# Kernel tuning notes

Measured on AMD Instinct MI355X. Metric: run time of the kernel, lower is better.

Reference implementation:

```python
import jax, jax.numpy as jnp
import numpy as np

B, S, E, R = 64, 2048, 256, 50


def setup_inputs() -> dict:
    key = jax.random.key(0)
    ks = jax.random.split(key, 22)
    n = lambda k, shp, s=0.05: (jax.random.normal(k, shp, jnp.float32) * s)
    d = {
        "encoder_o": jax.random.normal(ks[0], (B, S, E), jnp.float32),
        "h0": jax.random.normal(ks[1], (1, B, E), jnp.float32),
        "c0": jax.random.normal(ks[2], (1, B, E), jnp.float32),
        "r_in": jax.random.randint(ks[3], (B,), 0, R),
        "k1": jax.random.randint(ks[4], (B, 1), 0, S),
        "k2": jax.random.randint(ks[5], (B, 1), 0, S),
        "W_ih": n(ks[6], (4 * E, E)),
        "W_hh": n(ks[7], (4 * E, E)),
        "b_ih": n(ks[8], (4 * E,)),
        "b_hh": n(ks[9], (4 * E,)),
        "W_attn": n(ks[10], (E, 2 * E)),
        "b_attn": n(ks[11], (E,)),
        "W_conv": n(ks[12], (E, 2 * E, 3)),
        "b_conv": n(ks[13], (E,)),
        "sos_emb": n(ks[14], (1, E)),
        "rel_emb": n(ks[15], (R, E)),
        "W_rel": n(ks[16], (R, E)),
        "b_rel": n(ks[17], (R,)),
        "W_ent1": n(ks[18], (1, E)),
        "b_ent1": n(ks[19], (1,)),
        "W_ent2": n(ks[20], (1, E)),
        "b_ent2": n(ks[21], (1,)),
    }
    return d


def reference(encoder_o, h0, c0, r_in, k1, k2, W_ih, W_hh, b_ih, b_hh,
              W_attn, b_attn, W_conv, b_conv, sos_emb, rel_emb,
              W_rel, b_rel, W_ent1, b_ent1, W_ent2, b_ent2):
    Bx, Sx, Ex = encoder_o.shape

    def lstm_step(x, h, c):  # single decode step, x/h/c: [B,E]
        gates = x @ W_ih.T + h @ W_hh.T + (b_ih + b_hh)  # [B,4E]
        i, f, g, o = jnp.split(gates, 4, axis=-1)        # PyTorch gate order i,f,g,o
        c2 = jax.nn.sigmoid(f) * c + jax.nn.sigmoid(i) * jnp.tanh(g)
        h2 = jax.nn.sigmoid(o) * jnp.tanh(c2)
        return h2, c2

    def attend(q):  # Luong dot attention + tanh(linear(cat(mix,q))); q: [B,E]
        scores = jnp.einsum('be,bse->bs', q, encoder_o)
        attn = jax.nn.softmax(scores, axis=-1)
        mix = jnp.einsum('bs,bse->be', attn, encoder_o)
        comb = jnp.concatenate([mix, q], axis=-1)        # [B,2E]
        return jnp.tanh(comb @ W_attn.T + b_attn)

    def step(x, h, c):
        h2, c2 = lstm_step(x, h, c)
        return attend(h2), h2, c2

    kern = jnp.transpose(W_conv, (2, 1, 0))  # [3, 2E, E] for NWC/WIO

    def ent_heads(o):  # o: [B,E]
        vec = jnp.broadcast_to(o[:, None, :], (Bx, Sx, Ex))  # seq_and_vec
        feat = jnp.concatenate([encoder_o, vec], axis=-1)    # [B,S,2E]
        conv = jax.lax.conv_general_dilated(
            feat, kern, (1,), 'SAME',
            dimension_numbers=('NWC', 'WIO', 'NWC')) + b_conv
        conv = jax.nn.relu(conv)                             # [B,S,E]
        e1 = conv @ W_ent1.T + b_ent1                        # [B,S,1]
        e2 = conv @ W_ent2.T + b_ent2
        return e1, e2

    h, c = h0[0], c0[0]
    # t1: <sos> -> relation logits
    x = jnp.broadcast_to(sos_emb[0], (Bx, Ex))
    out1, h, c = step(x, h, c)
    t1_out = out1 @ W_rel.T + b_rel                          # [B,R]
    # t2: relation embedding -> entity-1 span heads
    out2, h, c = step(rel_emb[r_in], h, c)
    e1a, e2a = ent_heads(out2)
    # t3: gathered k1+k2 encoder vectors -> entity-2 span heads
    idx = jnp.arange(Bx)
    kk = encoder_o[idx, k1[:, 0]] + encoder_o[idx, k2[:, 0]]  # vectorized seq_gather
    out3, h, c = step(kk, h, c)
    e1b, e2b = ent_heads(out3)
    # pack outputs: [B, R + 4*S]
    return jnp.concatenate(
        [t1_out, e1a[..., 0], e2a[..., 0], e1b[..., 0], e2b[..., 0]], axis=1)
```

## Files before the change

kernel.cpp:

```cpp
#include <hip/hip_runtime.h>
#include <hip/hip_bf16.h>

#define EE 256
#define SS 2048
#define BB 64
#define RN 50
#define OSTR 8242
#define NCH 32

typedef __attribute__((ext_vector_type(4))) float vf4;
typedef __attribute__((ext_vector_type(8))) short s8v;
typedef __attribute__((ext_vector_type(4))) short s4v;
typedef __attribute__((ext_vector_type(4))) unsigned short u16x4;
typedef __attribute__((ext_vector_type(2))) unsigned int u32x2;
typedef __attribute__((ext_vector_type(4))) unsigned int u32x4;

__device__ __forceinline__ unsigned short f2bf(float f){
  __hip_bfloat16 h = __float2bfloat16(f);
  return *reinterpret_cast<unsigned short*>(&h);
}
__device__ __forceinline__ unsigned int f2bf2(float a, float b){
  __hip_bfloat162 h = __float22bfloat162_rn(make_float2(a, b));
  return *reinterpret_cast<unsigned int*>(&h);
}
__device__ __forceinline__ float sigm(float x){ return 1.0f/(1.0f + __expf(-x)); }
__device__ __forceinline__ float dot4(vf4 a, vf4 b){ return a.x*b.x + a.y*b.y + a.z*b.z + a.w*b.w; }

__device__ __forceinline__ vf4 mfma16(s4v a, s4v b, vf4 c){
#if __has_builtin(__builtin_amdgcn_mfma_f32_16x16x16bf16_1k)
  return __builtin_amdgcn_mfma_f32_16x16x16bf16_1k(a, b, c, 0, 0, 0);
#else
  vf4 d;
  asm volatile("v_mfma_f32_16x16x16_bf16 %0, %1, %2, %3\n\ts_nop 7\n\ts_nop 7"
               : "=v"(d) : "v"(a), "v"(b), "v"(c));
  return d;
#endif
}

__device__ __forceinline__ void gload_lds16(const void* g, void* l){
  __builtin_amdgcn_global_load_lds(
      (const __attribute__((address_space(1))) unsigned int*)g,
      (__attribute__((address_space(3))) unsigned int*)l, 16, 0, 0);
}

__global__ __launch_bounds__(256) void k_prep(
  const float* __restrict__ enc, const float* __restrict__ h0, const float* __restrict__ c0,
  const int* __restrict__ r_in, const int* __restrict__ k1, const int* __restrict__ k2,
  const float* __restrict__ sos, const float* __restrict__ rel,
  const float* __restrict__ W_conv,
  float* __restrict__ xT, float* __restrict__ hT0, float* __restrict__ cT,
  unsigned short* __restrict__ WT, unsigned short* __restrict__ Bp)
{
  int bid = blockIdx.x, t = threadIdx.x;
  if (bid < 256){
    int part = bid >> 6, b = bid & 63;
    if (part == 0){
      xT[(size_t)0*EE*BB + t*BB + b] = sos[t];
    } else if (part == 1){
      xT[(size_t)1*EE*BB + t*BB + b] = rel[r_in[b]*EE + t];
    } else if (part == 2){
      int i1 = k1[b], i2 = k2[b];
      xT[(size_t)2*EE*BB + t*BB + b] =
        enc[((size_t)b*SS + i1)*EE + t] + enc[((size_t)b*SS + i2)*EE + t];
    } else {
      hT0[t*BB + b] = h0[b*EE + t];
      cT [t*BB + b] = c0[b*EE + t];
    }
  } else if (bid < 512){
    int o = bid - 256;
    for (int r = t; r < 768; r += 256)
      WT[(size_t)r*EE + o] = f2bf(W_conv[(size_t)o*1536 + 768 + r]);
  } else {
    int gid = (bid - 512)*256 + t;
    int kc  = gid >> 10;
    int rem = gid & 1023;
    int ni  = rem >> 6;
    int l   = rem & 63;
    int o   = ni*16 + (l & 15);
    int kbase = kc*32 + ((l >> 4) << 3);
    u16x4 lo4, hi4;
    #pragma unroll
    for (int j=0;j<8;++j){
      int k = kbase + j; int ktap = k >> 8; int i = k & 255;
      unsigned short v = f2bf(W_conv[((size_t)o*512 + i)*3 + ktap]);
      if (j<4){ if(j==0)lo4.x=v; else if(j==1)lo4.y=v; else if(j==2)lo4.z=v; else lo4.w=v; }
      else    { if(j==4)hi4.x=v; else if(j==5)hi4.y=v; else if(j==6)hi4.z=v; else hi4.w=v; }
    }
    u16x4* dst = (u16x4*)(Bp + (size_t)gid*8);
    dst[0] = lo4; dst[1] = hi4;
  }
}

__global__ __launch_bounds__(256) void k_step(
  const float* __restrict__ hT_cur, const float* __restrict__ xT_st,
  const float* __restrict__ W_ih, const float* __restrict__ W_hh,
  const float* __restrict__ b_ih, const float* __restrict__ b_hh,
  float* __restrict__ cT, float* __restrict__ hT_next, float* __restrict__ hs_st)
{
  int e = blockIdx.x, tid = threadIdx.x;
  int w = tid >> 6, b = tid & 63;
  int grow = w*EE + e;
  const float* wh = W_hh + (size_t)grow*EE;
  const float* wi = W_ih + (size_t)grow*EE;
  float acc = b_ih[grow] + b_hh[grow];
  #pragma unroll 4
  for (int k4 = 0; k4 < EE/4; ++k4){
    vf4 wh4 = *(const vf4*)(wh + k4*4);
    vf4 wi4 = *(const vf4*)(wi + k4*4);
    int k = k4*4;
    acc += hT_cur[(k+0)*BB+b]*wh4.x + hT_cur[(k+1)*BB+b]*wh4.y
         + hT_cur[(k+2)*BB+b]*wh4.z + hT_cur[(k+3)*BB+b]*wh4.w;
    acc += xT_st[(k+0)*BB+b]*wi4.x + xT_st[(k+1)*BB+b]*wi4.y
         + xT_st[(k+2)*BB+b]*wi4.z + xT_st[(k+3)*BB+b]*wi4.w;
  }
  __shared__ float sm[4][BB];
  sm[w][b] = acc;
  __syncthreads();
  if (tid < BB){
    float iv = sm[0][tid], fv = sm[1][tid], gv = sm[2][tid], ov = sm[3][tid];
    float cprev = cT[e*BB + tid];
    float cn = sigm(fv)*cprev + sigm(iv)*tanhf(gv);
    float hn = sigm(ov)*tanhf(cn);
    cT[e*BB + tid] = cn;
    hT_next[e*BB + tid] = hn;
    hs_st[(size_t)tid*EE + e] = hn;
  }
}

__global__ __launch_bounds__(256, 2) void k_attend(
  const float* __restrict__ enc, const float* __restrict__ hs,
  float* __restrict__ mixc, float* __restrict__ stats,
  unsigned short* __restrict__ encb)
{
  int bid = blockIdx.x; int b = bid >> 5, ch = bid & 31;
  int tid = threadIdx.x, lane = tid & 63, wv = tid >> 6;
  __shared__ __align__(16) float rows[64*260];
  __shared__ float sc[3][64];
  __shared__ __align__(16) char smx[12288];
  float* hsm = (float*)smx;
  vf4 (*mpart)[3][64] = (vf4(*)[3][64])smx;

  const float* rowbase = enc + ((size_t)b*SS + ch*64)*EE;
  #pragma unroll
  for (int j=0;j<16;++j){
    int r = wv*16 + j;
    gload_lds16(rowbase + (size_t)r*EE + lane*4, (char*)rows + r*1040);
  }
  for (int i = tid; i < 3*EE; i += 256)
    hsm[i] = hs[((size_t)(i>>8)*BB + b)*EE + (i&255)];
  __syncthreads();

  {
    int r = tid >> 2, q = tid & 3;
    const vf4* rp = (const vf4*)(rows + r*260 + q*64);
    const vf4* q0 = (const vf4*)(hsm + 0*EE + q*64);
    const vf4* q1 = (const vf4*)(hsm + 1*EE + q*64);
    const vf4* q2 = (const vf4*)(hsm + 2*EE + q*64);
    int gs = ch*64 + r;
    char* ebase = encb ? ((char*)encb + ((size_t)b*SS + gs)*512 + q*128) : nullptr;
    int key = ((gs + 1) & 7) << 4;
    float a0=0.f, a1=0.f, a2=0.f;
    u32x2 prev;
    #pragma unroll
    for (int k=0;k<16;++k){
      vf4 ev = rp[k];
      a0 += dot4(ev, q0[k]);
      a1 += dot4(ev, q1[k]);
      a2 += dot4(ev, q2[k]);
      if (ebase){
        u32x2 pk; pk.x = f2bf2(ev.x, ev.y); pk.y = f2bf2(ev.z, ev.w);
        if (k & 1){
          u32x4 st4; st4.x = prev.x; st4.y = prev.y; st4.z = pk.x; st4.w = pk.y;
          *(u32x4*)(ebase + (((k>>1)*16) ^ key)) = st4;
        } else prev = pk;
      }
    }
    a0 += __shfl_xor(a0,1); a0 += __shfl_xor(a0,2);
    a1 += __shfl_xor(a1,1); a1 += __shfl_xor(a1,2);
    a2 += __shfl_xor(a2,1); a2 += __shfl_xor(a2,2);
    if (q == 0){ sc[0][r] = a0; sc[1][r] = a1; sc[2][r] = a2; }
  }
  __syncthreads();

  if (tid < 64){
    float s0 = sc[0][tid], s1 = sc[1][tid], s2 = sc[2][tid];
    float m0=s0, m1=s1, m2=s2;
    #pragma unroll
    for (int d=1; d<64; d<<=1){
      m0 = fmaxf(m0, __shfl_xor(m0,d));
      m1 = fmaxf(m1, __shfl_xor(m1,d));
      m2 = fmaxf(m2, __shfl_xor(m2,d));
    }
    float e0 = __expf(s0-m0), e1 = __expf(s1-m1), e2 = __expf(s2-m2);
    sc[0][tid]=e0; sc[1][tid]=e1; sc[2][tid]=e2;
    float l0=e0, l1=e1, l2=e2;
    #pragma unroll
    for (int d=1; d<64; d<<=1){
      l0 += __shfl_xor(l0,d); l1 += __shfl_xor(l1,d); l2 += __shfl_xor(l2,d);
    }
    if (tid == 0){
      int o0 = ((0*BB+b)*NCH + ch)*2; stats[o0]=m0; stats[o0+1]=l0;
      int o1 = ((1*BB+b)*NCH + ch)*2; stats[o1]=m1; stats[o1+1]=l1;
      int o2 = ((2*BB+b)*NCH + ch)*2; stats[o2]=m2; stats[o2+1]=l2;
    }
  }
  __syncthreads();

  {
    vf4 A0 = (vf4)0.0f, A1 = (vf4)0.0f, A2 = (vf4)0.0f;
    #pragma unroll 4
    for (int j=0;j<16;++j){
      int r = wv*16 + j;
      float w0 = sc[0][r], w1 = sc[1][r], w2 = sc[2][r];
      vf4 ev = *(const vf4*)(rows + r*260 + lane*4);
      A0 += ev*w0; A1 += ev*w1; A2 += ev*w2;
    }
    mpart[wv][0][lane]=A0; mpart[wv][1][lane]=A1; mpart[wv][2][lane]=A2;
  }
  __syncthreads();
  if (tid < 192){
    int q = tid >> 6, e4 = tid & 63;
    vf4 sum = mpart[0][q][e4] + mpart[1][q][e4] + mpart[2][q][e4] + mpart[3][q][e4];
    *(vf4*)(mixc + ((size_t)(q*BB+b)*NCH + ch)*EE + e4*4) = sum;
  }
}

__global__ __launch_bounds__(256) void k_post(
  const float* __restrict__ mixc, const float* __restrict__ hs,
  const float* __restrict__ stats,
  const float* __restrict__ W_attn, const float* __restrict__ b_attn,
  const float* __restrict__ W_rel, const float* __restrict__ b_rel,
  const unsigned short* __restrict__ WT, const float* __restrict__ b_conv,
  float* __restrict__ out, float* __restrict__ vv)
{
  int b = blockIdx.x, t = threadIdx.x;
  __shared__ float comb[3][2*EE];
  __shared__ float o1[EE], o2s[EE], o3s[EE];
  #pragma unroll
  for (int q=0;q<3;q++){
    float M = -1e30f;
    for (int c=0;c<NCH;c++) M = fmaxf(M, stats[((q*BB+b)*NCH + c)*2]);
    float L = 0.f, macc = 0.f;
    for (int c=0;c<NCH;c++){
      int o = ((q*BB+b)*NCH + c)*2;
      float e = __expf(stats[o]-M);
      L += stats[o+1]*e;
      macc += mixc[((size_t)(q*BB+b)*NCH + c)*EE + t] * e;
    }
    comb[q][t] = macc / L;
    comb[q][EE+t] = hs[((size_t)q*BB + b)*EE + t];
  }
  __syncthreads();
  float a0 = b_attn[t], a1 = a0, a2 = a0;
  const vf4* wr = (const vf4*)(W_attn + (size_t)t*2*EE);
  const vf4* c0v = (const vf4*)comb[0];
  const vf4* c1v = (const vf4*)comb[1];
  const vf4* c2v = (const vf4*)comb[2];
  #pragma unroll 4
  for (int k=0;k<2*EE/4;++k){
    vf4 w = wr[k];
    a0 += dot4(w, c0v[k]); a1 += dot4(w, c1v[k]); a2 += dot4(w, c2v[k]);
  }
  o1[t]=tanhf(a0); o2s[t]=tanhf(a1); o3s[t]=tanhf(a2);
  __syncthreads();
  if (t < RN){
    float acc = b_rel[t];
    const vf4* wrel = (const vf4*)(W_rel + (size_t)t*EE);
    const vf4* ov = (const vf4*)o1;
    for (int k=0;k<EE/4;++k) acc += dot4(wrel[k], ov[k]);
    out[(size_t)b*OSTR + t] = acc;
  }
  float va0=0,va1=0,va2=0, vb0=0,vb1=0,vb2=0;
  for (int i=0;i<EE;++i){
    float x2 = o2s[i], x3 = o3s[i];
    const unsigned short* wt = WT + (size_t)i*3*EE + t;
    float w0 = __uint_as_float(((unsigned int)wt[0]) << 16);
    float w1 = __uint_as_float(((unsigned int)wt[EE]) << 16);
    float w2 = __uint_as_float(((unsigned int)wt[2*EE]) << 16);
    va0 += x2*w0; va1 += x2*w1; va2 += x2*w2;
    vb0 += x3*w0; vb1 += x3*w1; vb2 += x3*w2;
  }
  float bc = b_conv[t];
  vv[((0*3+0)*BB + b)*EE + t] = va0+va1+va2+bc;
  vv[((0*3+1)*BB + b)*EE + t] = va1+va2+bc;
  vv[((0*3+2)*BB + b)*EE + t] = va0+va1+bc;
  vv[((1*3+0)*BB + b)*EE + t] = vb0+vb1+vb2+bc;
  vv[((1*3+1)*BB + b)*EE + t] = vb1+vb2+bc;
  vv[((1*3+2)*BB + b)*EE + t] = vb0+vb1+bc;
}

__global__ __launch_bounds__(256, 3) void k_conv(
  const float* __restrict__ enc, const unsigned short* __restrict__ encb,
  const unsigned short* __restrict__ Bp,
  const float* __restrict__ vv,
  const float* __restrict__ W_e1, const float* __restrict__ b_e1,
  const float* __restrict__ W_e2, const float* __restrict__ b_e2,
  float* __restrict__ out)
{
  int stile = blockIdx.x, b = blockIdx.y;
  int s0 = stile*64;
  int tid = threadIdx.x, lane = tid & 63, w = tid >> 6;
  int lo = lane & 15, hi = lane >> 4;
  __shared__ __align__(16) unsigned short Ab[66*256];
  __shared__ float part2[4][64][4];

  if (encb){
    const char* ebase = (const char*)encb + (size_t)b*SS*512;
    for (int base = 0; base < 66*32; base += 256){
      int idx = base + tid;
      if (idx < 66*32){
        int r = idx >> 5, c = idx & 31;
        int srow = s0 - 1 + r;
        srow = srow < 0 ? 0 : (srow > SS-1 ? SS-1 : srow);
        gload_lds16(ebase + (size_t)srow*512 + c*16, (char*)Ab + idx*16);
      }
    }
    __syncthreads();
    if (stile == 0 || stile == 31){
      if (stile == 0  && tid < 32) *(vf4*)((char*)Ab + tid*16) = (vf4)0.0f;
      if (stile == 31 && tid < 32) *(vf4*)((char*)Ab + 65*512 + tid*16) = (vf4)0.0f;
      __syncthreads();
    }
  } else {
    const float* eb = enc + (size_t)b*SS*EE;
    for (int idx = tid; idx < 66*64; idx += 256){
      int r = idx >> 6, c4 = idx & 63;
      int s = s0 - 1 + r;
      vf4 v = (vf4)0.0f;
      if (s >= 0 && s < SS) v = *(const vf4*)(eb + (size_t)s*EE + c4*4);
      u32x2 pk; pk.x = f2bf2(v.x, v.y); pk.y = f2bf2(v.z, v.w);
      int byte = (r*512 + c4*8) ^ ((r & 7) << 4);
      *(u32x2*)((char*)Ab + byte) = pk;
    }
    __syncthreads();
  }

  vf4 acc[4][4];
  #pragma unroll
  for (int oi=0;oi<4;++oi){
    #pragma unroll
    for (int si=0;si<4;++si) acc[oi][si] = (vf4)0.0f;
  }
  const s8v* Bp8 = (const s8v*)Bp;
  s8v bf[4], bfn[4];
  #pragma unroll
  for (int oi=0;oi<4;++oi) bf[oi] = Bp8[((0*16 + (w*4+oi)) << 6) + lane];

  for (int kc=0; kc<24; ++kc){
    int ktap = kc >> 3;
    int colb = ((kc & 7) << 6) + (hi << 4);
    s8v af[4];
    #pragma unroll
    for (int si=0;si<4;++si){
      int row = si*16 + lo + ktap;
      int byte = row*512 + (colb ^ ((row & 7) << 4));
      af[si] = *(const s8v*)((const char*)Ab + byte);
    }
    if (kc < 23){
      #pragma unroll
      for (int oi=0;oi<4;++oi) bfn[oi] = Bp8[(((kc+1)*16 + (w*4+oi)) << 6) + lane];
    }
    #pragma unroll
    for (int oi=0;oi<4;++oi){
      #pragma unroll
      for (int si=0;si<4;++si)
        acc[oi][si] = __builtin_amdgcn_mfma_f32_16x16x32_bf16(bf[oi], af[si], acc[oi][si], 0, 0, 0);
    }
    #pragma unroll
    for (int oi=0;oi<4;++oi) bf[oi] = bfn[oi];
  }

  bool firstTile = (s0 == 0), lastTile = (s0 + 64 == SS);
  vf4 vaI[4], vbI[4]; s4v aw[4];
  #pragma unroll
  for (int oi=0;oi<4;++oi){
    int o4 = w*64 + oi*16 + hi*4;
    vaI[oi] = *(const vf4*)(vv + ((0*3+0)*BB + b)*EE + o4);
    vbI[oi] = *(const vf4*)(vv + ((1*3+0)*BB + b)*EE + o4);
    vf4 w1 = *(const vf4*)(W_e1 + o4);
    vf4 w2 = *(const vf4*)(W_e2 + o4);
    float e0 = (lo==0) ? w1.x : ((lo==1) ? w2.x : 0.0f);
    float e1 = (lo==0) ? w1.y : ((lo==1) ? w2.y : 0.0f);
    float e2 = (lo==0) ? w1.z : ((lo==1) ? w2.z : 0.0f);
    float e3 = (lo==0) ? w1.w : ((lo==1) ? w2.w : 0.0f);
    u32x2 t; t.x = f2bf2(e0, e1); t.y = f2bf2(e2, e3);
    aw[oi] = __builtin_bit_cast(s4v, t);
  }
  #pragma unroll
  for (int si=0; si<4; ++si){
    vf4 Da = (vf4)0.0f, Db = (vf4)0.0f;
    #pragma unroll
    for (int oi=0; oi<4; ++oi){
      int o4 = w*64 + oi*16 + hi*4;
      vf4 c = acc[oi][si];
      vf4 va = vaI[oi], vb = vbI[oi];
      if (firstTile && si==0 && lo==0){
        va = *(const vf4*)(vv + ((0*3+1)*BB + b)*EE + o4);
        vb = *(const vf4*)(vv + ((1*3+1)*BB + b)*EE + o4);
      }
      if (lastTile && si==3 && lo==15){
        va = *(const vf4*)(vv + ((0*3+2)*BB + b)*EE + o4);
        vb = *(const vf4*)(vv + ((1*3+2)*BB + b)*EE + o4);
      }
      float a0 = fmaxf(c.x+va.x,0.f), a1 = fmaxf(c.y+va.y,0.f);
      float a2 = fmaxf(c.z+va.z,0.f), a3 = fmaxf(c.w+va.w,0.f);
      float b0 = fmaxf(c.x+vb.x,0.f), b1 = fmaxf(c.y+vb.y,0.f);
      float b2 = fmaxf(c.z+vb.z,0.f), b3 = fmaxf(c.w+vb.w,0.f);
      u32x2 ta; ta.x = f2bf2(a0,a1); ta.y = f2bf2(a2,a3);
      u32x2 tb; tb.x = f2bf2(b0,b1); tb.y = f2bf2(b2,b3);
      Da = mfma16(aw[oi], __builtin_bit_cast(s4v, ta), Da);
      Db = mfma16(aw[oi], __builtin_bit_cast(s4v, tb), Db);
    }
    if (hi == 0){
      vf4 pk; pk.x = Da.x; pk.y = Da.y; pk.z = Db.x; pk.w = Db.y;
      *(vf4*)&part2[w][si*16+lo][0] = pk;
    }
  }
  __syncthreads();
  {
    int s = tid >> 2, c = tid & 3;
    float r = part2[0][s][c] + part2[1][s][c] + part2[2][s][c] + part2[3][s][c];
    r += (c & 1) ? b_e2[0] : b_e1[0];
    out[(size_t)b*OSTR + RN + c*SS + (s0 + s)] = r;
  }
}

extern "C" void kernel_launch(void* const* d_in, const int* in_sizes, int n_in,
                              void* d_out, int out_size, void* d_ws, size_t ws_size,
                              hipStream_t stream)
{
  const float* enc   = (const float*)d_in[0];
  const float* h0    = (const float*)d_in[1];
  const float* c0    = (const float*)d_in[2];
  const int*   r_in  = (const int*)d_in[3];
  const int*   k1    = (const int*)d_in[4];
  const int*   k2    = (const int*)d_in[5];
  const float* W_ih  = (const float*)d_in[6];
  const float* W_hh  = (const float*)d_in[7];
  const float* b_ih  = (const float*)d_in[8];
  const float* b_hh  = (const float*)d_in[9];
  const float* W_attn= (const float*)d_in[10];
  const float* b_attn= (const float*)d_in[11];
  const float* W_conv= (const float*)d_in[12];
  const float* b_conv= (const float*)d_in[13];
  const float* sos   = (const float*)d_in[14];
  const float* rel   = (const float*)d_in[15];
  const float* W_rel = (const float*)d_in[16];
  const float* b_rel = (const float*)d_in[17];
  const float* W_e1  = (const float*)d_in[18];
  const float* b_e1  = (const float*)d_in[19];
  const float* W_e2  = (const float*)d_in[20];
  const float* b_e2  = (const float*)d_in[21];
  float* out = (float*)d_out;
  char* ws = (char*)d_ws;

  float* hs    = (float*)(ws);
  float* vv    = (float*)(ws + 196608);
  float* stats = (float*)(ws + 589824);
  float* mixc  = (float*)(ws + 638976);
  unsigned short* Bp = (unsigned short*)(ws + 6930432);
  float* xT    = (float*)(ws + 7323648);
  float* hTa   = (float*)(ws + 7520256);
  float* hTb   = (float*)(ws + 7585792);
  float* cT    = (float*)(ws + 7651328);
  unsigned short* WT = (unsigned short*)(ws + 7716864);
  size_t encb_off = 8110080;
  size_t need = encb_off + (size_t)BB*SS*EE*2;
  unsigned short* encb = (ws_size >= need) ? (unsigned short*)(ws + encb_off) : nullptr;

  hipLaunchKernelGGL(k_prep,  dim3(608), dim3(256), 0, stream,
                     enc,h0,c0,r_in,k1,k2,sos,rel,W_conv, xT,hTa,cT, WT,Bp);
  hipLaunchKernelGGL(k_step,  dim3(256), dim3(256), 0, stream,
                     hTa, xT + 0*EE*BB, W_ih,W_hh,b_ih,b_hh, cT, hTb, hs + 0*BB*EE);
  hipLaunchKernelGGL(k_step,  dim3(256), dim3(256), 0, stream,
                     hTb, xT + 1*EE*BB, W_ih,W_hh,b_ih,b_hh, cT, hTa, hs + 1*BB*EE);
  hipLaunchKernelGGL(k_step,  dim3(256), dim3(256), 0, stream,
                     hTa, xT + 2*EE*BB, W_ih,W_hh,b_ih,b_hh, cT, hTb, hs + 2*BB*EE);
  hipLaunchKernelGGL(k_attend,dim3(2048), dim3(256), 0, stream, enc, hs, mixc, stats, encb);
  hipLaunchKernelGGL(k_post,  dim3(64),  dim3(256), 0, stream,
                     mixc, hs, stats, W_attn,b_attn, W_rel,b_rel, WT, b_conv, out, vv);
  hipLaunchKernelGGL(k_conv,  dim3(32,64), dim3(256), 0, stream,
                     enc, encb, Bp, vv, W_e1,b_e1, W_e2,b_e2, out);
}
```

Before: 216.6 us.

## Drop LDS staging in attention kernel and widen post kernel to 1024 threads

The attention kernel no longer stages each 64-row encoder chunk in LDS (about 66 KB). It computes the scores straight from global memory with query vectors held in registers and a 16-lane shuffle reduction, then re-reads the rows from global for the mix pass and the bf16 encoder copy. This frees LDS so more blocks fit per CU, at the cost of reading the chunk from global twice, with the second read relying on cache hits. The post kernel now runs 1024 threads per batch row, spreading the three attention queries, a split-K conv-vector product and the relation logits across more threads to raise parallelism in a 64-block launch.

```diff
diff --git a/kernel.cpp b/kernel.cpp
--- a/kernel.cpp
+++ b/kernel.cpp
@@ -13,7 +13,6 @@
 typedef __attribute__((ext_vector_type(4))) short s4v;
 typedef __attribute__((ext_vector_type(4))) unsigned short u16x4;
 typedef __attribute__((ext_vector_type(2))) unsigned int u32x2;
-typedef __attribute__((ext_vector_type(4))) unsigned int u32x4;
 
 __device__ __forceinline__ unsigned short f2bf(float f){
   __hip_bfloat16 h = __float2bfloat16(f);
@@ -127,58 +126,43 @@
   }
 }
 
-__global__ __launch_bounds__(256, 2) void k_attend(
+__global__ __launch_bounds__(256) void k_attend(
   const float* __restrict__ enc, const float* __restrict__ hs,
   float* __restrict__ mixc, float* __restrict__ stats,
   unsigned short* __restrict__ encb)
 {
   int bid = blockIdx.x; int b = bid >> 5, ch = bid & 31;
   int tid = threadIdx.x, lane = tid & 63, wv = tid >> 6;
-  __shared__ __align__(16) float rows[64*260];
   __shared__ float sc[3][64];
-  __shared__ __align__(16) char smx[12288];
-  float* hsm = (float*)smx;
-  vf4 (*mpart)[3][64] = (vf4(*)[3][64])smx;
-
-  const float* rowbase = enc + ((size_t)b*SS + ch*64)*EE;
-  #pragma unroll
-  for (int j=0;j<16;++j){
-    int r = wv*16 + j;
-    gload_lds16(rowbase + (size_t)r*EE + lane*4, (char*)rows + r*1040);
-  }
-  for (int i = tid; i < 3*EE; i += 256)
-    hsm[i] = hs[((size_t)(i>>8)*BB + b)*EE + (i&255)];
-  __syncthreads();
+  __shared__ vf4 mpart[4][3][64];
+
+  const float* chunk = enc + ((size_t)b*SS + ch*64)*EE;
 
   {
-    int r = tid >> 2, q = tid & 3;
-    const vf4* rp = (const vf4*)(rows + r*260 + q*64);
-    const vf4* q0 = (const vf4*)(hsm + 0*EE + q*64);
-    const vf4* q1 = (const vf4*)(hsm + 1*EE + q*64);
-    const vf4* q2 = (const vf4*)(hsm + 2*EE + q*64);
-    int gs = ch*64 + r;
-    char* ebase = encb ? ((char*)encb + ((size_t)b*SS + gs)*512 + q*128) : nullptr;
-    int key = ((gs + 1) & 7) << 4;
-    float a0=0.f, a1=0.f, a2=0.f;
-    u32x2 prev;
-    #pragma unroll
-    for (int k=0;k<16;++k){
-      vf4 ev = rp[k];
-      a0 += dot4(ev, q0[k]);
-      a1 += dot4(ev, q1[k]);
-      a2 += dot4(ev, q2[k]);
-      if (ebase){
-        u32x2 pk; pk.x = f2bf2(ev.x, ev.y); pk.y = f2bf2(ev.z, ev.w);
-        if (k & 1){
-          u32x4 st4; st4.x = prev.x; st4.y = prev.y; st4.z = pk.x; st4.w = pk.y;
-          *(u32x4*)(ebase + (((k>>1)*16) ^ key)) = st4;
-        } else prev = pk;
-      }
-    }
-    a0 += __shfl_xor(a0,1); a0 += __shfl_xor(a0,2);
-    a1 += __shfl_xor(a1,1); a1 += __shfl_xor(a1,2);
-    a2 += __shfl_xor(a2,1); a2 += __shfl_xor(a2,2);
-    if (q == 0){ sc[0][r] = a0; sc[1][r] = a1; sc[2][r] = a2; }
+    int rs = lane >> 4, cg = lane & 15;
+    vf4 q0[4], q1[4], q2[4];
+    #pragma unroll
+    for (int v=0; v<4; ++v){
+      q0[v] = *(const vf4*)(hs + ((size_t)0*BB + b)*EE + cg*16 + v*4);
+      q1[v] = *(const vf4*)(hs + ((size_t)1*BB + b)*EE + cg*16 + v*4);
+      q2[v] = *(const vf4*)(hs + ((size_t)2*BB + b)*EE + cg*16 + v*4);
+    }
+    #pragma unroll
+    for (int i=0; i<4; ++i){
+      int r = wv*16 + i*4 + rs;
+      const vf4* rp = (const vf4*)(chunk + (size_t)r*EE + cg*16);
+      float a0=0.f, a1=0.f, a2=0.f;
+      #pragma unroll
+      for (int v=0; v<4; ++v){
+        vf4 ev = rp[v];
+        a0 += dot4(ev, q0[v]); a1 += dot4(ev, q1[v]); a2 += dot4(ev, q2[v]);
+      }
+      #pragma unroll
+      for (int d=1; d<16; d<<=1){
+        a0 += __shfl_xor(a0,d); a1 += __shfl_xor(a1,d); a2 += __shfl_xor(a2,d);
+      }
+      if (cg == 0){ sc[0][r]=a0; sc[1][r]=a1; sc[2][r]=a2; }
+    }
   }
   __syncthreads();
 
@@ -211,8 +195,14 @@
     #pragma unroll 4
     for (int j=0;j<16;++j){
       int r = wv*16 + j;
+      int gs = ch*64 + r;
+      vf4 ev = *(const vf4*)(chunk + (size_t)r*EE + lane*4);
+      if (encb){
+        u32x2 pk; pk.x = f2bf2(ev.x, ev.y); pk.y = f2bf2(ev.z, ev.w);
+        int key = ((gs + 1) & 7) << 4;
+        *(u32x2*)((char*)encb + ((size_t)b*SS + gs)*512 + ((lane*8) ^ key)) = pk;
+      }
       float w0 = sc[0][r], w1 = sc[1][r], w2 = sc[2][r];
-      vf4 ev = *(const vf4*)(rows + r*260 + lane*4);
       A0 += ev*w0; A1 += ev*w1; A2 += ev*w2;
     }
     mpart[wv][0][lane]=A0; mpart[wv][1][lane]=A1; mpart[wv][2][lane]=A2;
@@ -225,7 +215,7 @@
   }
 }
 
-__global__ __launch_bounds__(256) void k_post(
+__global__ __launch_bounds__(1024) void k_post(
   const float* __restrict__ mixc, const float* __restrict__ hs,
   const float* __restrict__ stats,
   const float* __restrict__ W_attn, const float* __restrict__ b_attn,
@@ -233,60 +223,78 @@
   const unsigned short* __restrict__ WT, const float* __restrict__ b_conv,
   float* __restrict__ out, float* __restrict__ vv)
 {
-  int b = blockIdx.x, t = threadIdx.x;
+  int b = blockIdx.x, tid = threadIdx.x;
   __shared__ float comb[3][2*EE];
-  __shared__ float o1[EE], o2s[EE], o3s[EE];
-  #pragma unroll
-  for (int q=0;q<3;q++){
+  __shared__ float ovs[3][EE];
+  __shared__ float vpart[2][6][EE];
+
+  if (tid < 768){
+    int q = tid >> 8, e = tid & 255;
     float M = -1e30f;
     for (int c=0;c<NCH;c++) M = fmaxf(M, stats[((q*BB+b)*NCH + c)*2]);
     float L = 0.f, macc = 0.f;
     for (int c=0;c<NCH;c++){
       int o = ((q*BB+b)*NCH + c)*2;
-      float e = __expf(stats[o]-M);
-      L += stats[o+1]*e;
-      macc += mixc[((size_t)(q*BB+b)*NCH + c)*EE + t] * e;
-    }
-    comb[q][t] = macc / L;
-    comb[q][EE+t] = hs[((size_t)q*BB + b)*EE + t];
-  }
-  __syncthreads();
-  float a0 = b_attn[t], a1 = a0, a2 = a0;
-  const vf4* wr = (const vf4*)(W_attn + (size_t)t*2*EE);
-  const vf4* c0v = (const vf4*)comb[0];
-  const vf4* c1v = (const vf4*)comb[1];
-  const vf4* c2v = (const vf4*)comb[2];
-  #pragma unroll 4
-  for (int k=0;k<2*EE/4;++k){
-    vf4 w = wr[k];
-    a0 += dot4(w, c0v[k]); a1 += dot4(w, c1v[k]); a2 += dot4(w, c2v[k]);
-  }
-  o1[t]=tanhf(a0); o2s[t]=tanhf(a1); o3s[t]=tanhf(a2);
-  __syncthreads();
-  if (t < RN){
-    float acc = b_rel[t];
-    const vf4* wrel = (const vf4*)(W_rel + (size_t)t*EE);
-    const vf4* ov = (const vf4*)o1;
-    for (int k=0;k<EE/4;++k) acc += dot4(wrel[k], ov[k]);
-    out[(size_t)b*OSTR + t] = acc;
-  }
-  float va0=0,va1=0,va2=0, vb0=0,vb1=0,vb2=0;
-  for (int i=0;i<EE;++i){
-    float x2 = o2s[i], x3 = o3s[i];
-    const unsigned short* wt = WT + (size_t)i*3*EE + t;
-    float w0 = __uint_as_float(((unsigned int)wt[0]) << 16);
-    float w1 = __uint_as_float(((unsigned int)wt[EE]) << 16);
-    float w2 = __uint_as_float(((unsigned int)wt[2*EE]) << 16);
-    va0 += x2*w0; va1 += x2*w1; va2 += x2*w2;
-    vb0 += x3*w0; vb1 += x3*w1; vb2 += x3*w2;
-  }
-  float bc = b_conv[t];
-  vv[((0*3+0)*BB + b)*EE + t] = va0+va1+va2+bc;
-  vv[((0*3+1)*BB + b)*EE + t] = va1+va2+bc;
-  vv[((0*3+2)*BB + b)*EE + t] = va0+va1+bc;
-  vv[((1*3+0)*BB + b)*EE + t] = vb0+vb1+vb2+bc;
-  vv[((1*3+1)*BB + b)*EE + t] = vb1+vb2+bc;
-  vv[((1*3+2)*BB + b)*EE + t] = vb0+vb1+bc;
+      float ee = __expf(stats[o]-M);
+      L += stats[o+1]*ee;
+      macc += mixc[((size_t)(q*BB+b)*NCH + c)*EE + e] * ee;
+    }
+    comb[q][e] = macc / L;
+    comb[q][EE+e] = hs[((size_t)q*BB + b)*EE + e];
+  }
+  __syncthreads();
+  if (tid < 768){
+    int q = tid >> 8, e = tid & 255;
+    float a = b_attn[e];
+    const vf4* wr = (const vf4*)(W_attn + (size_t)e*2*EE);
+    const vf4* cv = (const vf4*)comb[q];
+    #pragma unroll 4
+    for (int k=0;k<2*EE/4;++k) a += dot4(wr[k], cv[k]);
+    ovs[q][e] = tanhf(a);
+  }
+  __syncthreads();
+  if (tid < 512){
+    int half = tid >> 8, o = tid & 255;
+    float va0=0,va1=0,va2=0, vb0=0,vb1=0,vb2=0;
+    int i0 = half*128;
+    for (int i=i0; i<i0+128; ++i){
+      float x2 = ovs[1][i], x3 = ovs[2][i];
+      const unsigned short* wt = WT + (size_t)i*3*EE + o;
+      float w0 = __uint_as_float(((unsigned int)wt[0]) << 16);
+      float w1 = __uint_as_float(((unsigned int)wt[EE]) << 16);
+      float w2 = __uint_as_float(((unsigned int)wt[2*EE]) << 16);
+      va0 += x2*w0; va1 += x2*w1; va2 += x2*w2;
+      vb0 += x3*w0; vb1 += x3*w1; vb2 += x3*w2;
+    }
+    vpart[half][0][o]=va0; vpart[half][1][o]=va1; vpart[half][2][o]=va2;
+    vpart[half][3][o]=vb0; vpart[half][4][o]=vb1; vpart[half][5][o]=vb2;
+  } else if (tid < 576){
+    int t = tid - 512;
+    if (t < RN){
+      float acc = b_rel[t];
+      const vf4* wrel = (const vf4*)(W_rel + (size_t)t*EE);
+      const vf4* ov = (const vf4*)ovs[0];
+      for (int k=0;k<EE/4;++k) acc += dot4(wrel[k], ov[k]);
+      out[(size_t)b*OSTR + t] = acc;
+    }
+  }
+  __syncthreads();
+  if (tid < 256){
+    int o = tid;
+    float va0 = vpart[0][0][o]+vpart[1][0][o];
+    float va1 = vpart[0][1][o]+vpart[1][1][o];
+    float va2 = vpart[0][2][o]+vpart[1][2][o];
+    float vb0 = vpart[0][3][o]+vpart[1][3][o];
+    float vb1 = vpart[0][4][o]+vpart[1][4][o];
+    float vb2 = vpart[0][5][o]+vpart[1][5][o];
+    float bc = b_conv[o];
+    vv[((0*3+0)*BB + b)*EE + o] = va0+va1+va2+bc;
+    vv[((0*3+1)*BB + b)*EE + o] = va1+va2+bc;
+    vv[((0*3+2)*BB + b)*EE + o] = va0+va1+bc;
+    vv[((1*3+0)*BB + b)*EE + o] = vb0+vb1+vb2+bc;
+    vv[((1*3+1)*BB + b)*EE + o] = vb1+vb2+bc;
+    vv[((1*3+2)*BB + b)*EE + o] = vb0+vb1+bc;
+  }
 }
 
 __global__ __launch_bounds__(256, 3) void k_conv(
@@ -477,7 +485,7 @@
   hipLaunchKernelGGL(k_step,  dim3(256), dim3(256), 0, stream,
                      hTa, xT + 2*EE*BB, W_ih,W_hh,b_ih,b_hh, cT, hTb, hs + 2*BB*EE);
   hipLaunchKernelGGL(k_attend,dim3(2048), dim3(256), 0, stream, enc, hs, mixc, stats, encb);
-  hipLaunchKernelGGL(k_post,  dim3(64),  dim3(256), 0, stream,
+  hipLaunchKernelGGL(k_post,  dim3(64),  dim3(1024), 0, stream,
                      mixc, hs, stats, W_attn,b_attn, W_rel,b_rel, WT, b_conv, out, vv);
   hipLaunchKernelGGL(k_conv,  dim3(32,64), dim3(256), 0, stream,
                      enc, encb, Bp, vv, W_e1,b_e1, W_e2,b_e2, out);
```

Measured after the change: 224.7 us. 1.04x slower.

## Keep encoder chunk in registers instead of LDS staging in attend kernel

Applied to the files above, without the earlier changes.

The attend kernel now loads each thread's slice of the 64-row encoder chunk directly into registers. The score, softmax-weighted mix and bf16 copy are all computed from those registers instead of from a large LDS buffer. Dot-product and mix reductions move to cross-lane shuffles, and each wave recomputes the softmax locally, which drops one block barrier. This frees most shared memory and avoids the LDS round trip, at the cost of much higher register use and many extra shuffle instructions.

```diff
diff --git a/kernel.cpp b/kernel.cpp
--- a/kernel.cpp
+++ b/kernel.cpp
@@ -127,63 +127,63 @@
   }
 }
 
-__global__ __launch_bounds__(256, 2) void k_attend(
+__global__ __launch_bounds__(256) void k_attend(
   const float* __restrict__ enc, const float* __restrict__ hs,
   float* __restrict__ mixc, float* __restrict__ stats,
   unsigned short* __restrict__ encb)
 {
   int bid = blockIdx.x; int b = bid >> 5, ch = bid & 31;
   int tid = threadIdx.x, lane = tid & 63, wv = tid >> 6;
-  __shared__ __align__(16) float rows[64*260];
+  int rs = lane >> 4, cg = lane & 15;
+  __shared__ float qsm[3][EE];
   __shared__ float sc[3][64];
-  __shared__ __align__(16) char smx[12288];
-  float* hsm = (float*)smx;
-  vf4 (*mpart)[3][64] = (vf4(*)[3][64])smx;
-
-  const float* rowbase = enc + ((size_t)b*SS + ch*64)*EE;
-  #pragma unroll
-  for (int j=0;j<16;++j){
-    int r = wv*16 + j;
-    gload_lds16(rowbase + (size_t)r*EE + lane*4, (char*)rows + r*1040);
+  __shared__ vf4 mpart[4][3][64];
+
+  const float* chunk = enc + ((size_t)b*SS + ch*64)*EE;
+
+  vf4 dat[4][4];
+  #pragma unroll
+  for (int i=0;i<4;++i){
+    const vf4* rp = (const vf4*)(chunk + (size_t)(wv*16 + i*4 + rs)*EE + cg*16);
+    #pragma unroll
+    for (int v=0;v<4;++v) dat[i][v] = rp[v];
   }
   for (int i = tid; i < 3*EE; i += 256)
-    hsm[i] = hs[((size_t)(i>>8)*BB + b)*EE + (i&255)];
+    qsm[i>>8][i&255] = hs[((size_t)(i>>8)*BB + b)*EE + (i&255)];
   __syncthreads();
 
   {
-    int r = tid >> 2, q = tid & 3;
-    const vf4* rp = (const vf4*)(rows + r*260 + q*64);
-    const vf4* q0 = (const vf4*)(hsm + 0*EE + q*64);
-    const vf4* q1 = (const vf4*)(hsm + 1*EE + q*64);
-    const vf4* q2 = (const vf4*)(hsm + 2*EE + q*64);
-    int gs = ch*64 + r;
-    char* ebase = encb ? ((char*)encb + ((size_t)b*SS + gs)*512 + q*128) : nullptr;
-    int key = ((gs + 1) & 7) << 4;
-    float a0=0.f, a1=0.f, a2=0.f;
-    u32x2 prev;
-    #pragma unroll
-    for (int k=0;k<16;++k){
-      vf4 ev = rp[k];
-      a0 += dot4(ev, q0[k]);
-      a1 += dot4(ev, q1[k]);
-      a2 += dot4(ev, q2[k]);
-      if (ebase){
-        u32x2 pk; pk.x = f2bf2(ev.x, ev.y); pk.y = f2bf2(ev.z, ev.w);
-        if (k & 1){
-          u32x4 st4; st4.x = prev.x; st4.y = prev.y; st4.z = pk.x; st4.w = pk.y;
-          *(u32x4*)(ebase + (((k>>1)*16) ^ key)) = st4;
-        } else prev = pk;
+    vf4 q0[4], q1[4], q2[4];
+    #pragma unroll
+    for (int v=0;v<4;++v){
+      q0[v] = *(const vf4*)(qsm[0] + cg*16 + v*4);
+      q1[v] = *(const vf4*)(qsm[1] + cg*16 + v*4);
+      q2[v] = *(const vf4*)(qsm[2] + cg*16 + v*4);
+    }
+    #pragma unroll
+    for (int i=0;i<4;++i){
+      float a0=0.f, a1=0.f, a2=0.f;
+      #pragma unroll
+      for (int v=0;v<4;++v){
+        a0 += dot4(dat[i][v], q0[v]);
+        a1 += dot4(dat[i][v], q1[v]);
+        a2 += dot4(dat[i][v], q2[v]);
       }
-    }
-    a0 += __shfl_xor(a0,1); a0 += __shfl_xor(a0,2);
-    a1 += __shfl_xor(a1,1); a1 += __shfl_xor(a1,2);
-    a2 += __shfl_xor(a2,1); a2 += __shfl_xor(a2,2);
-    if (q == 0){ sc[0][r] = a0; sc[1][r] = a1; sc[2][r] = a2; }
-  }
-  __syncthreads();
-
-  if (tid < 64){
-    float s0 = sc[0][tid], s1 = sc[1][tid], s2 = sc[2][tid];
+      #pragma unroll
+      for (int d=1; d<16; d<<=1){
+        a0 += __shfl_xor(a0,d); a1 += __shfl_xor(a1,d); a2 += __shfl_xor(a2,d);
+      }
+      if (cg == 0){
+        int r = wv*16 + i*4 + rs;
+        sc[0][r]=a0; sc[1][r]=a1; sc[2][r]=a2;
+      }
+    }
+  }
+  __syncthreads();
+
+  float e0, e1, e2;
+  {
+    float s0 = sc[0][lane], s1 = sc[1][lane], s2 = sc[2][lane];
     float m0=s0, m1=s1, m2=s2;
     #pragma unroll
     for (int d=1; d<64; d<<=1){
@@ -191,8 +191,7 @@
       m1 = fmaxf(m1, __shfl_xor(m1,d));
       m2 = fmaxf(m2, __shfl_xor(m2,d));
     }
-    float e0 = __expf(s0-m0), e1 = __expf(s1-m1), e2 = __expf(s2-m2);
-    sc[0][tid]=e0; sc[1][tid]=e1; sc[2][tid]=e2;
+    e0 = __expf(s0-m0); e1 = __expf(s1-m1); e2 = __expf(s2-m2);
     float l0=e0, l1=e1, l2=e2;
     #pragma unroll
     for (int d=1; d<64; d<<=1){
@@ -204,18 +203,50 @@
       int o2 = ((2*BB+b)*NCH + ch)*2; stats[o2]=m2; stats[o2+1]=l2;
     }
   }
-  __syncthreads();
-
-  {
-    vf4 A0 = (vf4)0.0f, A1 = (vf4)0.0f, A2 = (vf4)0.0f;
-    #pragma unroll 4
-    for (int j=0;j<16;++j){
-      int r = wv*16 + j;
-      float w0 = sc[0][r], w1 = sc[1][r], w2 = sc[2][r];
-      vf4 ev = *(const vf4*)(rows + r*260 + lane*4);
-      A0 += ev*w0; A1 += ev*w1; A2 += ev*w2;
-    }
-    mpart[wv][0][lane]=A0; mpart[wv][1][lane]=A1; mpart[wv][2][lane]=A2;
+
+  vf4 A0[4], A1[4], A2[4];
+  #pragma unroll
+  for (int v=0;v<4;++v){ A0[v]=(vf4)0.0f; A1[v]=(vf4)0.0f; A2[v]=(vf4)0.0f; }
+  #pragma unroll
+  for (int i=0;i<4;++i){
+    int r = wv*16 + i*4 + rs;
+    int gs = ch*64 + r;
+    float w0 = __shfl(e0, r), w1 = __shfl(e1, r), w2 = __shfl(e2, r);
+    if (encb){
+      int key = ((gs + 1) & 7) << 4;
+      char* base = (char*)encb + ((size_t)b*SS + gs)*512;
+      u32x4 lo4, hi4;
+      lo4.x = f2bf2(dat[i][0].x, dat[i][0].y); lo4.y = f2bf2(dat[i][0].z, dat[i][0].w);
+      lo4.z = f2bf2(dat[i][1].x, dat[i][1].y); lo4.w = f2bf2(dat[i][1].z, dat[i][1].w);
+      hi4.x = f2bf2(dat[i][2].x, dat[i][2].y); hi4.y = f2bf2(dat[i][2].z, dat[i][2].w);
+      hi4.z = f2bf2(dat[i][3].x, dat[i][3].y); hi4.w = f2bf2(dat[i][3].z, dat[i][3].w);
+      *(u32x4*)(base + ((cg*32     ) ^ key)) = lo4;
+      *(u32x4*)(base + ((cg*32 + 16) ^ key)) = hi4;
+    }
+    #pragma unroll
+    for (int v=0;v<4;++v){
+      A0[v] += dat[i][v]*w0; A1[v] += dat[i][v]*w1; A2[v] += dat[i][v]*w2;
+    }
+  }
+  #pragma unroll
+  for (int v=0;v<4;++v){
+    #pragma unroll
+    for (int d=16; d<64; d<<=1){
+      A0[v].x += __shfl_xor(A0[v].x,d); A0[v].y += __shfl_xor(A0[v].y,d);
+      A0[v].z += __shfl_xor(A0[v].z,d); A0[v].w += __shfl_xor(A0[v].w,d);
+      A1[v].x += __shfl_xor(A1[v].x,d); A1[v].y += __shfl_xor(A1[v].y,d);
+      A1[v].z += __shfl_xor(A1[v].z,d); A1[v].w += __shfl_xor(A1[v].w,d);
+      A2[v].x += __shfl_xor(A2[v].x,d); A2[v].y += __shfl_xor(A2[v].y,d);
+      A2[v].z += __shfl_xor(A2[v].z,d); A2[v].w += __shfl_xor(A2[v].w,d);
+    }
+  }
+  if (rs == 0){
+    #pragma unroll
+    for (int v=0;v<4;++v){
+      mpart[wv][0][cg*4+v] = A0[v];
+      mpart[wv][1][cg*4+v] = A1[v];
+      mpart[wv][2][cg*4+v] = A2[v];
+    }
   }
   __syncthreads();
   if (tid < 192){
```

Measured after the change: 201.2 us. 7.1% less time.
